# Performance work log

Hardware: AMD Instinct MI355X
Metric: run time of the kernel (lower is better)

Reference implementation:

```python
import jax, jax.numpy as jnp
import numpy as np

B, CIN, COUT, H, W, KS, PAD = 8, 64, 128, 32, 32, 3, 1
OH, OW = H, W  # stride 1, pad 1, dilation 1 -> same spatial size
QMIN, QMAX = -128, 127


def setup_inputs() -> dict:
    key = jax.random.key(0)
    k1, k2, k3 = jax.random.split(key, 3)
    x = jax.random.normal(k1, (B, CIN, H, W), jnp.float32)
    weight = jax.random.normal(k2, (COUT, CIN, KS, KS), jnp.float32) * 0.05
    bias = jax.random.normal(k3, (COUT,), jnp.float32) * 0.01
    # exact int8 product LUT: lut[a+128, b+128] = a*b (the 'approximate multiplier' table)
    q = jnp.arange(QMIN, QMAX + 1, dtype=jnp.int32)  # [256]
    lut = q[:, None] * q[None, :]                     # [256,256] int32
    # gradient LUT: d(a*b)/da = b, d(a*b)/db = a
    gradient_lut = jnp.stack([
        jnp.broadcast_to(q[None, :], (256, 256)),
        jnp.broadcast_to(q[:, None], (256, 256)),
    ]).astype(jnp.float32)                            # [2,256,256]
    T_feature = jnp.ones((1,), jnp.float32)
    T_weight = jnp.ones((1,), jnp.float32)
    return {"x": x, "weight": weight, "bias": bias, "lut": lut,
            "gradient_lut": gradient_lut, "T_feature": T_feature, "T_weight": T_weight}


def _quantize(v, T):
    scale = 127.0 / T
    return jnp.clip(jnp.round(v * scale), QMIN, QMAX).astype(jnp.int32)


def _lut_conv(xq, wq, lut):
    """LUT-based int8 conv. xq [B,CIN,H,W] int32 in [-128,127], wq [COUT,CIN,KS,KS]."""
    xp = jnp.pad(xq, ((0, 0), (0, 0), (PAD, PAD), (PAD, PAD)))
    # im2col: 9 structurally-distinct kernel offsets (fixed small loop)
    patches = jnp.stack([xp[:, :, i:i + OH, j:j + OW]
                         for i in range(KS) for j in range(KS)], axis=2)  # [B,CIN,9,OH,OW]
    K = CIN * KS * KS
    cols = patches.transpose(0, 3, 4, 1, 2).reshape(B * OH * OW, K)  # [P,K]
    wf = wq.reshape(COUT, K)                                         # [COUT,K]
    lut_flat = lut.reshape(-1)

    def step(acc, xs):
        xk, wk = xs  # xk [P], wk [COUT]
        idx = (xk[:, None] + 128) * 256 + (wk[None, :] + 128)  # [P,COUT]
        return acc + lut_flat[idx], None

    acc0 = jnp.zeros((B * OH * OW, COUT), jnp.int32)
    acc, _ = jax.lax.scan(step, acc0, (cols.T, wf.T))  # scan over K patch elems
    return acc.reshape(B, OH, OW, COUT).transpose(0, 3, 1, 2)  # [B,COUT,OH,OW]


def reference(x, weight, bias, lut, gradient_lut, T_feature, T_weight):
    # EMA threshold update (update_T_func), detached scalars in the original
    Tf = 0.95 * T_feature[0] + 0.05 * jnp.max(jnp.abs(x))
    Tw = 0.95 * T_weight[0] + 0.05 * jnp.max(jnp.abs(weight))
    xq = _quantize(x, Tf)
    wq = _quantize(weight, Tw)
    acc = _lut_conv(xq, wq, lut).astype(jnp.float32)
    out = acc * ((Tf / 127.0) * (Tw / 127.0)) + bias[None, :, None, None]
    return out
```

## Files before the change

### kernel.cpp

```cpp
#include <hip/hip_runtime.h>
#include <cstdint>

#define BATCH 8
#define CIN 64
#define COUT 128
#define HH 32
#define WW 32
#define PH 34
#define PW 34

typedef int v4i __attribute__((ext_vector_type(4)));

#define WS_TF 0
#define WS_TW 1
#define WS_PART 16
#define XPAD_OFF 4096
#define WFRAG_OFF (4096 + BATCH * PH * PW * CIN)

__global__ __launch_bounds__(256) void absmax_partial(const float* __restrict__ x,
                                                      const float* __restrict__ w,
                                                      float* __restrict__ partials) {
    float m = 0.0f;
    if (blockIdx.x < 128) {
        const float4* p = (const float4*)x;
        int base = blockIdx.x * 1024 + threadIdx.x;
        #pragma unroll
        for (int k = 0; k < 4; ++k) {
            float4 v = p[base + k * 256];
            m = fmaxf(m, fmaxf(fmaxf(fabsf(v.x), fabsf(v.y)), fmaxf(fabsf(v.z), fabsf(v.w))));
        }
    } else {
        const float4* p = (const float4*)w;
        int wb = blockIdx.x - 128;
        int base = wb * 1152 + threadIdx.x;
        int end = (wb + 1) * 1152;
        #pragma unroll
        for (int k = 0; k < 5; ++k) {
            int i = base + k * 256;
            if (i < end) {
                float4 v = p[i];
                m = fmaxf(m, fmaxf(fmaxf(fabsf(v.x), fabsf(v.y)), fmaxf(fabsf(v.z), fabsf(v.w))));
            }
        }
    }
    #pragma unroll
    for (int off = 32; off > 0; off >>= 1)
        m = fmaxf(m, __shfl_xor(m, off, 64));
    __shared__ float sm[4];
    int wave = threadIdx.x >> 6;
    if ((threadIdx.x & 63) == 0) sm[wave] = m;
    __syncthreads();
    if (threadIdx.x == 0)
        partials[WS_PART + blockIdx.x] = fmaxf(fmaxf(sm[0], sm[1]), fmaxf(sm[2], sm[3]));
}

__device__ __forceinline__ int quant1(float v, float scale) {
    float q = rintf(v * scale);
    q = fminf(fmaxf(q, -128.0f), 127.0f);
    return (int)q;
}

#define NBX 578
#define NBW 72
__global__ __launch_bounds__(256) void quant_pack(const float* __restrict__ x,
                                                  const float* __restrict__ w,
                                                  const float* __restrict__ Tf_in,
                                                  const float* __restrict__ Tw_in,
                                                  float* __restrict__ ws_f32,
                                                  uint8_t* __restrict__ xpad,
                                                  uint8_t* __restrict__ wfrag) {
    int lane = threadIdx.x & 63;
    if (blockIdx.x < NBX) {
        float m = fmaxf(ws_f32[WS_PART + lane], ws_f32[WS_PART + 64 + lane]);
        #pragma unroll
        for (int off = 32; off > 0; off >>= 1)
            m = fmaxf(m, __shfl_xor(m, off, 64));
        float a = 0.95f * Tf_in[0];
        float b = 0.05f * m;
        float Tf = a + b;
        if (blockIdx.x == 0 && threadIdx.x == 0) ws_f32[WS_TF] = Tf;
        float scale = 127.0f / Tf;

        int tid = blockIdx.x * 256 + threadIdx.x;
        int idx4 = tid * 4;
        int ci0 = idx4 & 63;
        int rest = idx4 >> 6;
        int iw = rest % PW;
        int t2 = rest / PW;
        int ih = t2 % PH;
        int bb = t2 / PH;
        unsigned pack = 0;
        if (ih >= 1 && ih <= HH && iw >= 1 && iw <= WW) {
            int h = ih - 1, ww_ = iw - 1;
            #pragma unroll
            for (int c = 0; c < 4; ++c) {
                float v = x[((bb * CIN + ci0 + c) * HH + h) * WW + ww_];
                int q = quant1(v, scale);
                pack |= ((unsigned)(q & 255)) << (8 * c);
            }
        }
        ((unsigned*)xpad)[tid] = pack;
    } else {
        float m = ws_f32[WS_PART + 128 + (lane & 15)];
        #pragma unroll
        for (int off = 32; off > 0; off >>= 1)
            m = fmaxf(m, __shfl_xor(m, off, 64));
        float a = 0.95f * Tw_in[0];
        float b = 0.05f * m;
        float Tw = a + b;
        if (blockIdx.x == NBX && threadIdx.x == 0) ws_f32[WS_TW] = Tw;
        float scale = 127.0f / Tw;

        int tid = (blockIdx.x - NBX) * 256 + threadIdx.x;
        int idx4 = tid * 4;
        int j0 = idx4 & 15;
        int ln = (idx4 >> 4) & 63;
        int f  = idx4 >> 10;
        int nt8 = f & 7;
        int t = f >> 3;
        int kh = t / 3;
        int kw = t - kh * 3;
        int co = nt8 * 16 + (ln & 15);
        int ci0 = (ln >> 4) * 16 + j0;
        unsigned pack = 0;
        #pragma unroll
        for (int c = 0; c < 4; ++c) {
            float v = w[((co * CIN + ci0 + c) * 3 + kh) * 3 + kw];
            int q = quant1(v, scale);
            pack |= ((unsigned)(q & 255)) << (8 * c);
        }
        ((unsigned*)wfrag)[tid] = pack;
    }
}

__global__ __launch_bounds__(256) void conv_mfma(const uint8_t* __restrict__ xpad,
                                                 const uint8_t* __restrict__ wfrag,
                                                 const float* __restrict__ bias,
                                                 const float* __restrict__ ws_f32,
                                                 float* __restrict__ out) {
    int mb = blockIdx.x;
    int b = mb >> 5;
    int oh = mb & 31;
    int wave = threadIdx.x >> 6;
    int lane = threadIdx.x & 63;
    int mt = wave & 1;
    int nh = wave >> 1;
    int row = lane & 15;
    int quad = lane >> 4;

    v4i acc[4];
    #pragma unroll
    for (int nt = 0; nt < 4; ++nt) acc[nt] = (v4i){0, 0, 0, 0};

    const uint8_t* xbase = xpad + (((b * PH + oh) * PW) + mt * 16 + row) * CIN + quad * 16;

    #pragma unroll
    for (int t = 0; t < 9; ++t) {
        const int kh = t / 3, kw = t % 3;
        v4i afrag = *(const v4i*)(xbase + (kh * PW + kw) * CIN);
        #pragma unroll
        for (int nt = 0; nt < 4; ++nt) {
            v4i bfrag = *(const v4i*)(wfrag + (((t * 8 + nh * 4 + nt) * 64) + lane) * 16);
            acc[nt] = __builtin_amdgcn_mfma_i32_16x16x64_i8(afrag, bfrag, acc[nt], 0, 0, 0);
        }
    }

    float Tf = ws_f32[WS_TF];
    float Tw = ws_f32[WS_TW];
    float s = (Tf / 127.0f) * (Tw / 127.0f);
    int ow0 = mt * 16 + quad * 4;
    #pragma unroll
    for (int nt = 0; nt < 4; ++nt) {
        int co = nh * 64 + nt * 16 + row;
        float bb = bias[co];
        float4 o;
        o.x = (float)acc[nt][0] * s + bb;
        o.y = (float)acc[nt][1] * s + bb;
        o.z = (float)acc[nt][2] * s + bb;
        o.w = (float)acc[nt][3] * s + bb;
        *(float4*)(out + (((b * COUT + co) * HH + oh) * WW) + ow0) = o;
    }
}

extern "C" void kernel_launch(void* const* d_in, const int* in_sizes, int n_in,
                              void* d_out, int out_size, void* d_ws, size_t ws_size,
                              hipStream_t stream) {
    const float* x        = (const float*)d_in[0];
    const float* weight   = (const float*)d_in[1];
    const float* bias     = (const float*)d_in[2];
    const float* T_feature = (const float*)d_in[5];
    const float* T_weight  = (const float*)d_in[6];

    float*   ws_f32 = (float*)d_ws;
    uint8_t* xpad   = (uint8_t*)d_ws + XPAD_OFF;
    uint8_t* wfrag  = (uint8_t*)d_ws + WFRAG_OFF;

    absmax_partial<<<144, 256, 0, stream>>>(x, weight, ws_f32);
    quant_pack<<<NBX + NBW, 256, 0, stream>>>(x, weight, T_feature, T_weight,
                                              ws_f32, xpad, wfrag);
    conv_mfma<<<256, 256, 0, stream>>>(xpad, wfrag, bias, ws_f32, (float*)d_out);
}
```

Measured before the change: 76.37 us.

## Transpose input quantization through LDS, zero only halo, split conv across more blocks

The input quantize-pack stage now reads x with coalesced float4 loads per (batch,row), packs to int8, and transposes through shared memory into the padded NHWC buffer. The halo is zeroed by separate dedicated blocks instead of every padded element being computed. Before, each thread gathered four strided channel values, giving uncoalesced reads. The conv kernel is split into twice as many blocks, each handling half the output channels, to give the GPU more parallelism. The cost is that each input fragment is loaded twice across blocks.

```diff
diff --git a/kernel.cpp b/kernel.cpp
--- a/kernel.cpp
+++ b/kernel.cpp
@@ -54,14 +54,15 @@
         partials[WS_PART + blockIdx.x] = fmaxf(fmaxf(sm[0], sm[1]), fmaxf(sm[2], sm[3]));
 }
 
-__device__ __forceinline__ int quant1(float v, float scale) {
+__device__ __forceinline__ unsigned quantb(float v, float scale) {
     float q = rintf(v * scale);
     q = fminf(fmaxf(q, -128.0f), 127.0f);
-    return (int)q;
-}
-
-#define NBX 578
-#define NBW 72
+    return ((unsigned)(int)q) & 255u;
+}
+
+#define QB_X 256
+#define QB_W 72
+#define QB_Z 66
 __global__ __launch_bounds__(256) void quant_pack(const float* __restrict__ x,
                                                   const float* __restrict__ w,
                                                   const float* __restrict__ Tf_in,
@@ -69,98 +70,119 @@
                                                   float* __restrict__ ws_f32,
                                                   uint8_t* __restrict__ xpad,
                                                   uint8_t* __restrict__ wfrag) {
-    int lane = threadIdx.x & 63;
-    if (blockIdx.x < NBX) {
+    int blk = blockIdx.x;
+    int t = threadIdx.x;
+    int lane = t & 63;
+
+    if (blk < QB_X) {
         float m = fmaxf(ws_f32[WS_PART + lane], ws_f32[WS_PART + 64 + lane]);
         #pragma unroll
         for (int off = 32; off > 0; off >>= 1)
             m = fmaxf(m, __shfl_xor(m, off, 64));
         float a = 0.95f * Tf_in[0];
-        float b = 0.05f * m;
-        float Tf = a + b;
-        if (blockIdx.x == 0 && threadIdx.x == 0) ws_f32[WS_TF] = Tf;
+        float bt = 0.05f * m;
+        float Tf = a + bt;
+        if (blk == 0 && t == 0) ws_f32[WS_TF] = Tf;
         float scale = 127.0f / Tf;
 
-        int tid = blockIdx.x * 256 + threadIdx.x;
-        int idx4 = tid * 4;
-        int ci0 = idx4 & 63;
-        int rest = idx4 >> 6;
-        int iw = rest % PW;
-        int t2 = rest / PW;
-        int ih = t2 % PH;
-        int bb = t2 / PH;
-        unsigned pack = 0;
-        if (ih >= 1 && ih <= HH && iw >= 1 && iw <= WW) {
-            int h = ih - 1, ww_ = iw - 1;
-            #pragma unroll
-            for (int c = 0; c < 4; ++c) {
-                float v = x[((bb * CIN + ci0 + c) * HH + h) * WW + ww_];
-                int q = quant1(v, scale);
-                pack |= ((unsigned)(q & 255)) << (8 * c);
-            }
-        }
-        ((unsigned*)xpad)[tid] = pack;
-    } else {
+        int b = blk >> 5, h = blk & 31;
+        const float4* x4 = (const float4*)x;
+        __shared__ unsigned lds[CIN * 9];
+        #pragma unroll
+        for (int k = 0; k < 2; ++k) {
+            int f = t + k * 256;
+            int ci = f >> 3, wq = f & 7;
+            float4 v = x4[(b * CIN + ci) * 256 + h * 8 + wq];
+            unsigned pack = quantb(v.x, scale) | (quantb(v.y, scale) << 8) |
+                            (quantb(v.z, scale) << 16) | (quantb(v.w, scale) << 24);
+            lds[ci * 9 + wq] = pack;
+        }
+        __syncthreads();
+        const uint8_t* ldsb = (const uint8_t*)lds;
+        unsigned* orow = (unsigned*)(xpad + (((b * PH) + (h + 1)) * PW + 1) * CIN);
+        #pragma unroll
+        for (int k = 0; k < 2; ++k) {
+            int o = t + k * 256;
+            int ww_ = o >> 4, c4 = o & 15;
+            unsigned d = (unsigned)ldsb[(c4 * 4 + 0) * 36 + ww_]
+                       | ((unsigned)ldsb[(c4 * 4 + 1) * 36 + ww_] << 8)
+                       | ((unsigned)ldsb[(c4 * 4 + 2) * 36 + ww_] << 16)
+                       | ((unsigned)ldsb[(c4 * 4 + 3) * 36 + ww_] << 24);
+            orow[o] = d;
+        }
+    } else if (blk < QB_X + QB_W) {
         float m = ws_f32[WS_PART + 128 + (lane & 15)];
         #pragma unroll
         for (int off = 32; off > 0; off >>= 1)
             m = fmaxf(m, __shfl_xor(m, off, 64));
         float a = 0.95f * Tw_in[0];
-        float b = 0.05f * m;
-        float Tw = a + b;
-        if (blockIdx.x == NBX && threadIdx.x == 0) ws_f32[WS_TW] = Tw;
+        float bt = 0.05f * m;
+        float Tw = a + bt;
+        if (blk == QB_X && t == 0) ws_f32[WS_TW] = Tw;
         float scale = 127.0f / Tw;
 
-        int tid = (blockIdx.x - NBX) * 256 + threadIdx.x;
+        int tid = (blk - QB_X) * 256 + t;
         int idx4 = tid * 4;
         int j0 = idx4 & 15;
         int ln = (idx4 >> 4) & 63;
         int f  = idx4 >> 10;
-        int nt8 = f & 7;
-        int t = f >> 3;
-        int kh = t / 3;
-        int kw = t - kh * 3;
-        int co = nt8 * 16 + (ln & 15);
+        int g = f & 7;
+        int tap = f >> 3;
+        int kh = tap / 3, kw = tap - kh * 3;
+        int co = g * 16 + (ln & 15);
         int ci0 = (ln >> 4) * 16 + j0;
         unsigned pack = 0;
         #pragma unroll
         for (int c = 0; c < 4; ++c) {
             float v = w[((co * CIN + ci0 + c) * 3 + kh) * 3 + kw];
-            int q = quant1(v, scale);
-            pack |= ((unsigned)(q & 255)) << (8 * c);
+            pack |= quantb(v, scale) << (8 * c);
         }
         ((unsigned*)wfrag)[tid] = pack;
-    }
-}
-
-__global__ __launch_bounds__(256) void conv_mfma(const uint8_t* __restrict__ xpad,
-                                                 const uint8_t* __restrict__ wfrag,
-                                                 const float* __restrict__ bias,
-                                                 const float* __restrict__ ws_f32,
-                                                 float* __restrict__ out) {
-    int mb = blockIdx.x;
+    } else {
+        int j = (blk - QB_X - QB_W) * 256 + t;
+        int p = j >> 4, c4 = j & 15;
+        int b = p / 132;
+        int r = p - b * 132;
+        int ih, iw;
+        if (r < 34)      { ih = 0;          iw = r; }
+        else if (r < 68) { ih = PH - 1;     iw = r - 34; }
+        else if (r < 100){ ih = r - 68 + 1; iw = 0; }
+        else             { ih = r - 100 + 1; iw = PW - 1; }
+        ((unsigned*)xpad)[((b * PH + ih) * PW + iw) * 16 + c4] = 0u;
+    }
+}
+
+__global__ __launch_bounds__(256, 2) void conv_mfma(const uint8_t* __restrict__ xpad,
+                                                    const uint8_t* __restrict__ wfrag,
+                                                    const float* __restrict__ bias,
+                                                    const float* __restrict__ ws_f32,
+                                                    float* __restrict__ out) {
+    int blk = blockIdx.x;
+    int nb = blk & 1;
+    int mb = blk >> 1;
     int b = mb >> 5;
     int oh = mb & 31;
     int wave = threadIdx.x >> 6;
     int lane = threadIdx.x & 63;
     int mt = wave & 1;
-    int nh = wave >> 1;
+    int nh2 = wave >> 1;
     int row = lane & 15;
     int quad = lane >> 4;
 
-    v4i acc[4];
+    v4i acc[2];
+    acc[0] = (v4i){0, 0, 0, 0};
+    acc[1] = (v4i){0, 0, 0, 0};
+
+    const uint8_t* xbase = xpad + (((b * PH + oh) * PW) + mt * 16 + row) * CIN + quad * 16;
+
     #pragma unroll
-    for (int nt = 0; nt < 4; ++nt) acc[nt] = (v4i){0, 0, 0, 0};
-
-    const uint8_t* xbase = xpad + (((b * PH + oh) * PW) + mt * 16 + row) * CIN + quad * 16;
-
-    #pragma unroll
-    for (int t = 0; t < 9; ++t) {
-        const int kh = t / 3, kw = t % 3;
+    for (int tp = 0; tp < 9; ++tp) {
+        const int kh = tp / 3, kw = tp % 3;
         v4i afrag = *(const v4i*)(xbase + (kh * PW + kw) * CIN);
         #pragma unroll
-        for (int nt = 0; nt < 4; ++nt) {
-            v4i bfrag = *(const v4i*)(wfrag + (((t * 8 + nh * 4 + nt) * 64) + lane) * 16);
+        for (int nt = 0; nt < 2; ++nt) {
+            int g = nb * 4 + nh2 * 2 + nt;
+            v4i bfrag = *(const v4i*)(wfrag + (((tp * 8 + g) * 64) + lane) * 16);
             acc[nt] = __builtin_amdgcn_mfma_i32_16x16x64_i8(afrag, bfrag, acc[nt], 0, 0, 0);
         }
     }
@@ -170,8 +192,9 @@
     float s = (Tf / 127.0f) * (Tw / 127.0f);
     int ow0 = mt * 16 + quad * 4;
     #pragma unroll
-    for (int nt = 0; nt < 4; ++nt) {
-        int co = nh * 64 + nt * 16 + row;
+    for (int nt = 0; nt < 2; ++nt) {
+        int g = nb * 4 + nh2 * 2 + nt;
+        int co = g * 16 + row;
         float bb = bias[co];
         float4 o;
         o.x = (float)acc[nt][0] * s + bb;
@@ -196,7 +219,7 @@
     uint8_t* wfrag  = (uint8_t*)d_ws + WFRAG_OFF;
 
     absmax_partial<<<144, 256, 0, stream>>>(x, weight, ws_f32);
-    quant_pack<<<NBX + NBW, 256, 0, stream>>>(x, weight, T_feature, T_weight,
-                                              ws_f32, xpad, wfrag);
-    conv_mfma<<<256, 256, 0, stream>>>(xpad, wfrag, bias, ws_f32, (float*)d_out);
-}
+    quant_pack<<<QB_X + QB_W + QB_Z, 256, 0, stream>>>(x, weight, T_feature, T_weight,
+                                                       ws_f32, xpad, wfrag);
+    conv_mfma<<<512, 256, 0, stream>>>(xpad, wfrag, bias, ws_f32, (float*)d_out);
+}
```

New measurement: 75.00 us. About the same (-1.8%).
